# Kernel optimization log

Hardware: AMD Instinct MI355X
Metric: run time of the kernel (lower is better)

Reference implementation:

```python
import jax, jax.numpy as jnp
import numpy as np
import math

B, T, C, NH = 8, 1024, 768, 12
HD = C // NH
EPS = 1e-5

def layer_norm(x, g, b):
    mu = jnp.mean(x, axis=-1, keepdims=True)
    var = jnp.mean(jnp.square(x - mu), axis=-1, keepdims=True)
    return (x - mu) * jax.lax.rsqrt(var + EPS) * g + b

def setup_inputs() -> dict:
    key = jax.random.key(0)
    ks = jax.random.split(key, 10)
    s = lambda n: 1.0 / math.sqrt(n)
    return {
        "x": jax.random.normal(ks[0], (B, T, C), jnp.float32),
        "attn_mask": jax.random.randint(ks[1], (B, T), 0, 2, jnp.int32),
        "ln1_g": jnp.ones((C,), jnp.float32),
        "ln1_b": jnp.zeros((C,), jnp.float32),
        "W_attn": jax.random.normal(ks[2], (C, 3 * C), jnp.float32) * s(C),
        "b_attn": jnp.zeros((3 * C,), jnp.float32),
        "W_proj": jax.random.normal(ks[3], (C, C), jnp.float32) * s(C),
        "b_proj": jnp.zeros((C,), jnp.float32),
        "ln2_g": jnp.ones((C,), jnp.float32),
        "ln2_b": jnp.zeros((C,), jnp.float32),
        "W_fc": jax.random.normal(ks[4], (C, 4 * C), jnp.float32) * s(C),
        "b_fc": jnp.zeros((4 * C,), jnp.float32),
        "W_fc2": jax.random.normal(ks[5], (4 * C, C), jnp.float32) * s(4 * C),
        "b_fc2": jnp.zeros((C,), jnp.float32),
    }

def reference(x, attn_mask, ln1_g, ln1_b, W_attn, b_attn, W_proj, b_proj,
              ln2_g, ln2_b, W_fc, b_fc, W_fc2, b_fc2):
    # --- attention branch ---
    h = layer_norm(x, ln1_g, ln1_b)                     # [B,T,C]
    qkv = h @ W_attn + b_attn                           # [B,T,3C]
    q, k, v = jnp.split(qkv, 3, axis=-1)
    q = q.reshape(B, T, NH, HD).transpose(0, 2, 1, 3)   # [B,H,T,D]
    k = k.reshape(B, T, NH, HD).transpose(0, 2, 1, 3)
    v = v.reshape(B, T, NH, HD).transpose(0, 2, 1, 3)
    attn = jnp.einsum('bhqd,bhkd->bhqk', q, k) * (1.0 / math.sqrt(HD))
    mask = attn_mask[:, None, None, :]                  # [B,1,1,T] key-padding
    attn = jnp.where(mask == 0, -jnp.inf, attn)
    attn = jax.nn.softmax(attn, axis=-1)
    o = jnp.einsum('bhqk,bhkd->bhqd', attn, v)          # [B,H,T,D]
    o = o.transpose(0, 2, 1, 3).reshape(B, T, C)
    x = x + (o @ W_proj + b_proj)
    # --- MLP branch ---
    h2 = layer_norm(x, ln2_g, ln2_b)
    h2 = jax.nn.gelu(h2 @ W_fc + b_fc, approximate=True)
    x = x + (h2 @ W_fc2 + b_fc2)
    return x
```

## Files before the change

### kernel.cpp

```cpp
#include <hip/hip_runtime.h>
#include <hip/hip_bf16.h>
#include <math.h>

constexpr int kB  = 8;
constexpr int kT  = 1024;
constexpr int kC  = 768;
constexpr int kNH = 12;
constexpr int kHD = 64;
constexpr int kM  = kB * kT;
constexpr int k3C = 3 * kC;
constexpr int k4C = 4 * kC;

typedef __bf16 bf16x8 __attribute__((ext_vector_type(8)));
typedef float  f32x4  __attribute__((ext_vector_type(4)));
typedef unsigned short u16x8 __attribute__((ext_vector_type(8)));

__device__ inline void gload_lds16(const void* g, void* l) {
  __builtin_amdgcn_global_load_lds(
      (const __attribute__((address_space(1))) void*)g,
      (__attribute__((address_space(3))) void*)l, 16, 0, 0);
}

__device__ inline float ldx(const float* p) { return *p; }
__device__ inline float ldx(const __hip_bfloat16* p) { return __bfloat162float(*p); }

template <typename TIN>
__global__ __launch_bounds__(256) void ln_kernel(
    const TIN* __restrict__ x, const float* __restrict__ g,
    const float* __restrict__ bta, __hip_bfloat16* __restrict__ out)
{
  __shared__ float red[4];
  int row = blockIdx.x;
  int tid = threadIdx.x;
  const TIN* xr = x + (size_t)row * kC;
  float v0 = ldx(xr + tid), v1 = ldx(xr + tid + 256), v2 = ldx(xr + tid + 512);

  float s = v0 + v1 + v2;
#pragma unroll
  for (int off = 32; off; off >>= 1) s += __shfl_xor(s, off);
  if ((tid & 63) == 0) red[tid >> 6] = s;
  __syncthreads();
  float mu = (red[0] + red[1] + red[2] + red[3]) * (1.0f / kC);

  float d0 = v0 - mu, d1 = v1 - mu, d2 = v2 - mu;
  float q = d0 * d0 + d1 * d1 + d2 * d2;
#pragma unroll
  for (int off = 32; off; off >>= 1) q += __shfl_xor(q, off);
  __syncthreads();
  if ((tid & 63) == 0) red[tid >> 6] = q;
  __syncthreads();
  float var = (red[0] + red[1] + red[2] + red[3]) * (1.0f / kC);
  float inv = rsqrtf(var + 1e-5f);

  __hip_bfloat16* orow = out + (size_t)row * kC;
  orow[tid]       = __float2bfloat16(d0 * inv * g[tid]       + bta[tid]);
  orow[tid + 256] = __float2bfloat16(d1 * inv * g[tid + 256] + bta[tid + 256]);
  orow[tid + 512] = __float2bfloat16(d2 * inv * g[tid + 512] + bta[tid + 512]);
}

__global__ __launch_bounds__(256) void transpose_cast(
    const float* __restrict__ W, __hip_bfloat16* __restrict__ WT, int K, int N)
{
  __shared__ __hip_bfloat16 t[64][65];
  int k0 = blockIdx.y * 64, n0 = blockIdx.x * 64;
  int tid = threadIdx.x;
#pragma unroll
  for (int it = 0; it < 16; ++it) {
    int e = it * 256 + tid;
    int r = e >> 6, c = e & 63;
    t[r][c] = __float2bfloat16(W[(size_t)(k0 + r) * N + n0 + c]);
  }
  __syncthreads();
#pragma unroll
  for (int it = 0; it < 16; ++it) {
    int e = it * 256 + tid;
    int nr = e >> 6, kc = e & 63;
    WT[(size_t)(n0 + nr) * K + k0 + kc] = t[kc][nr];
  }
}

__global__ __launch_bounds__(256) void v_transpose(
    const __hip_bfloat16* __restrict__ qkv, __hip_bfloat16* __restrict__ vt)
{
  __shared__ __hip_bfloat16 tile[64][80];
  int b = blockIdx.z, h = blockIdx.y, t0 = blockIdx.x * 64;
  int tid = threadIdx.x;
  const __hip_bfloat16* vb = qkv + (size_t)(b * kT) * k3C + 2 * kC + h * kHD;
#pragma unroll
  for (int it = 0; it < 2; ++it) {
    int e = it * 256 + tid;
    int r = e >> 3, c8 = (e & 7) * 8;
    *(u16x8*)&tile[r][c8] = *(const u16x8*)(vb + (size_t)(t0 + r) * k3C + c8);
  }
  __syncthreads();
  __hip_bfloat16* vrow = vt + (size_t)(b * kNH + h) * kHD * kT;
#pragma unroll
  for (int it = 0; it < 2; ++it) {
    int e = it * 256 + tid;
    int d = e >> 3, k8 = (e & 7) * 8;
    u16x8 u;
#pragma unroll
    for (int m = 0; m < 8; ++m)
      u[m] = *(const unsigned short*)&tile[k8 + m][d];
    *(u16x8*)(vrow + (size_t)d * kT + t0 + k8) = u;
  }
}

__device__ inline float gelu_fast(float c) {
  float t = 0.7978845608028654f * (c + 0.044715f * c * c * c);
  float e = exp2f(t * 2.8853900817779268f);
  float th = 1.0f - 2.0f * __builtin_amdgcn_rcpf(e + 1.0f);
  return 0.5f * c * (1.0f + th);
}

template <int MODE>
__global__ __launch_bounds__(256) void gemm_bf16(
    const __hip_bfloat16* __restrict__ A,
    const __hip_bfloat16* __restrict__ WT,
    const float* __restrict__ bias,
    const void* __restrict__ Rv,
    void* __restrict__ outv, int M, int N, int K)
{
  __shared__ __align__(16) __hip_bfloat16 As[2][128 * 64];
  __shared__ __align__(16) __hip_bfloat16 Bs[2][128 * 64];
  const int tid  = threadIdx.x;
  const int lane = tid & 63, wid = tid >> 6;
  const int wr = wid >> 1, wc = wid & 1;
  const int r16 = lane & 15, g = lane >> 4;

  const int nwg = gridDim.x * gridDim.y;
  const int bid = blockIdx.y * gridDim.x + blockIdx.x;
  const int swz = (bid & 7) * (nwg >> 3) + (bid >> 3);
  const int m0 = (swz / gridDim.x) * 128;
  const int n0 = (swz % gridDim.x) * 128;

  const __hip_bfloat16* Abase = A  + (size_t)m0 * K;
  const __hip_bfloat16* Bbase = WT + (size_t)n0 * K;

  f32x4 acc[4][4] = {};

  auto stage = [&](int t, int buf) {
    const __hip_bfloat16* Ap = Abase + t * 64;
    const __hip_bfloat16* Bp = Bbase + t * 64;
#pragma unroll
    for (int it = 0; it < 4; ++it) {
      int e = it * 256 + tid;
      int row = e >> 3, ch = (e & 7) ^ (row & 7);
      char* la = (char*)&As[buf][0] + (it * 4096 + (tid & ~63) * 16);
      char* lb = (char*)&Bs[buf][0] + (it * 4096 + (tid & ~63) * 16);
      gload_lds16(Ap + (size_t)row * K + ch * 8, la);
      gload_lds16(Bp + (size_t)row * K + ch * 8, lb);
    }
  };

  auto compute = [&](const char* Ab, const char* Bb) {
#pragma unroll
    for (int s = 0; s < 2; ++s) {
      bf16x8 af[4], bf[4];
#pragma unroll
      for (int i = 0; i < 4; ++i) {
        int ar = wr * 64 + i * 16 + r16;
        af[i] = *(const bf16x8*)(Ab + ar * 128 + (((s * 4 + g) ^ (ar & 7)) << 4));
        int br = wc * 64 + i * 16 + r16;
        bf[i] = *(const bf16x8*)(Bb + br * 128 + (((s * 4 + g) ^ (br & 7)) << 4));
      }
#pragma unroll
      for (int i = 0; i < 4; ++i)
#pragma unroll
        for (int j = 0; j < 4; ++j)
          acc[i][j] = __builtin_amdgcn_mfma_f32_16x16x32_bf16(af[i], bf[j],
                                                              acc[i][j], 0, 0, 0);
    }
  };

  const int NT = K >> 6;
  stage(0, 0);
  __syncthreads();

  for (int t = 0; t < NT; t += 2) {
    stage(t + 1, 1);
    compute((const char*)&As[0][0], (const char*)&Bs[0][0]);
    __syncthreads();
    if (t + 2 < NT) stage(t + 2, 0);
    compute((const char*)&As[1][0], (const char*)&Bs[1][0]);
    __syncthreads();
  }

  const int r0 = m0 + wr * 64 + g * 4;
  const int c0 = n0 + wc * 64 + r16;
#pragma unroll
  for (int i = 0; i < 4; ++i) {
#pragma unroll
    for (int j = 0; j < 4; ++j) {
      int col = c0 + j * 16;
      float bv = bias[col];
#pragma unroll
      for (int q = 0; q < 4; ++q) {
        int row = r0 + i * 16 + q;
        float c = acc[i][j][q] + bv;
        if (MODE == 3) {
          c += ((const float*)Rv)[(size_t)row * N + col];
          ((__hip_bfloat16*)outv)[(size_t)row * N + col] = __float2bfloat16(c);
        } else if (MODE == 4) {
          c += __bfloat162float(((const __hip_bfloat16*)Rv)[(size_t)row * N + col]);
          ((float*)outv)[(size_t)row * N + col] = c;
        } else {
          if (MODE == 2) c = gelu_fast(c);
          ((__hip_bfloat16*)outv)[(size_t)row * N + col] = __float2bfloat16(c);
        }
      }
    }
  }
}

__global__ __launch_bounds__(256) void attn_mfma(
    const __hip_bfloat16* __restrict__ qkv,
    const __hip_bfloat16* __restrict__ vt,
    const int* __restrict__ mask,
    __hip_bfloat16* __restrict__ o)
{
  __shared__ __align__(16) __hip_bfloat16 Ks[2][64 * 64];
  __shared__ __align__(16) __hip_bfloat16 Vs[2][64 * 64];
  __shared__ __align__(16) __hip_bfloat16 Ps[4 * 16 * 64];

  const int b = blockIdx.z, h = blockIdx.y, q0 = blockIdx.x * 64;
  const int tid = threadIdx.x, lane = tid & 63, wid = tid >> 6;
  const int r16 = lane & 15, g = lane >> 4;
  const size_t rs = k3C;
  const __hip_bfloat16* qb = qkv + (size_t)(b * kT) * rs + h * kHD;
  const __hip_bfloat16* kb = qb + kC;
  const __hip_bfloat16* vtb = vt + (size_t)(b * kNH + h) * kHD * kT;
  const int* mrow = mask + b * kT;
  constexpr float kSc = 0.125f * 1.4426950408889634f;

  auto stage = [&](int t, int buf) {
#pragma unroll
    for (int it = 0; it < 2; ++it) {
      int e = it * 256 + tid;
      int row = e >> 3, ch = (e & 7) ^ (row & 7);
      char* lk = (char*)&Ks[buf][0] + (it * 4096 + (tid & ~63) * 16);
      char* lv = (char*)&Vs[buf][0] + (it * 4096 + (tid & ~63) * 16);
      gload_lds16(kb + (size_t)(t * 64 + row) * rs + ch * 8, lk);
      gload_lds16(vtb + (size_t)row * kT + t * 64 + ch * 8, lv);
    }
  };

  bf16x8 qf[2];
  {
    const __hip_bfloat16* qr = qb + (size_t)(q0 + wid * 16 + r16) * rs;
#pragma unroll
    for (int s = 0; s < 2; ++s) qf[s] = *(const bf16x8*)(qr + s * 32 + g * 8);
  }
  stage(0, 0);
  unsigned long long km = 0;
#pragma unroll
  for (int t = 0; t < 16; ++t)
#pragma unroll
    for (int j = 0; j < 4; ++j)
      if (mrow[t * 64 + 16 * j + r16] != 0)
        km |= 1ull << (t * 4 + j);
  __syncthreads();

  f32x4 o_acc[4] = {};
  float l_part[4] = {0.f, 0.f, 0.f, 0.f};
  __hip_bfloat16* Pw = Ps + wid * 1024;

  for (int t = 0; t < 16; ++t) {
    const int buf = t & 1;
    if (t + 1 < 16) stage(t + 1, buf ^ 1);

    const char* Kb = (const char*)&Ks[buf][0];
    const char* Vb = (const char*)&Vs[buf][0];

    f32x4 sa[4] = {};
#pragma unroll
    for (int j = 0; j < 4; ++j) {
#pragma unroll
      for (int s = 0; s < 2; ++s) {
        int kr = 16 * j + r16;
        bf16x8 kf = *(const bf16x8*)(Kb + kr * 128 +
                                     (((s * 4 + g) ^ (kr & 7)) << 4));
        sa[j] = __builtin_amdgcn_mfma_f32_16x16x32_bf16(qf[s], kf, sa[j], 0, 0, 0);
      }
    }

#pragma unroll
    for (int r = 0; r < 4; ++r) {
      float p[4];
#pragma unroll
      for (int j = 0; j < 4; ++j) {
        float pj = exp2f(sa[j][r] * kSc);
        p[j] = ((km >> (t * 4 + j)) & 1ull) ? pj : 0.f;
      }
      l_part[r] += (p[0] + p[1]) + (p[2] + p[3]);
      int q = g * 4 + r;
      char* pwq = (char*)Pw + q * 128 + (r16 & 7) * 2;
#pragma unroll
      for (int j = 0; j < 4; ++j) {
        int chn = ((j << 1) | (r16 >> 3)) ^ (q & 7);
        *(__hip_bfloat16*)(pwq + (chn << 4)) = __float2bfloat16(p[j]);
      }
    }

    asm volatile("s_waitcnt lgkmcnt(0)" ::: "memory");
    __builtin_amdgcn_sched_barrier(0);

#pragma unroll
    for (int s = 0; s < 2; ++s) {
      bf16x8 pf = *(const bf16x8*)((const char*)Pw + r16 * 128 +
                                   (((s * 4 + g) ^ (r16 & 7)) << 4));
#pragma unroll
      for (int db = 0; db < 4; ++db) {
        int vr = 16 * db + r16;
        bf16x8 vf = *(const bf16x8*)(Vb + vr * 128 +
                                     (((s * 4 + g) ^ (vr & 7)) << 4));
        o_acc[db] = __builtin_amdgcn_mfma_f32_16x16x32_bf16(pf, vf, o_acc[db], 0, 0, 0);
      }
    }
    __syncthreads();
  }

#pragma unroll
  for (int r = 0; r < 4; ++r) {
    float l = l_part[r];
#pragma unroll
    for (int off = 8; off; off >>= 1) l += __shfl_xor(l, off);
    float inv = 1.f / l;
    size_t row = (size_t)(b * kT) + q0 + wid * 16 + g * 4 + r;
#pragma unroll
    for (int db = 0; db < 4; ++db)
      o[row * kC + h * kHD + 16 * db + r16] = __float2bfloat16(o_acc[db][r] * inv);
  }
}

extern "C" void kernel_launch(void* const* d_in, const int* in_sizes, int n_in,
                              void* d_out, int out_size, void* d_ws, size_t ws_size,
                              hipStream_t stream) {
  const float* x      = (const float*)d_in[0];
  const int*   amask  = (const int*)  d_in[1];
  const float* ln1_g  = (const float*)d_in[2];
  const float* ln1_b  = (const float*)d_in[3];
  const float* W_attn = (const float*)d_in[4];
  const float* b_attn = (const float*)d_in[5];
  const float* W_proj = (const float*)d_in[6];
  const float* b_proj = (const float*)d_in[7];
  const float* ln2_g  = (const float*)d_in[8];
  const float* ln2_b  = (const float*)d_in[9];
  const float* W_fc   = (const float*)d_in[10];
  const float* b_fc   = (const float*)d_in[11];
  const float* W_fc2  = (const float*)d_in[12];
  const float* b_fc2  = (const float*)d_in[13];
  float* out = (float*)d_out;

  char* ws = (char*)d_ws;
  __hip_bfloat16* h_bf    = (__hip_bfloat16*)(ws);
  __hip_bfloat16* qkv_bf  = (__hip_bfloat16*)(ws + (size_t)16 * 1024 * 1024);
  __hip_bfloat16* fc_bf   = qkv_bf;
  __hip_bfloat16* wt_attn = (__hip_bfloat16*)(ws + (size_t)68 * 1024 * 1024);
  __hip_bfloat16* wt_proj = (__hip_bfloat16*)(ws + (size_t)72 * 1024 * 1024);
  __hip_bfloat16* wt_fc   = (__hip_bfloat16*)(ws + (size_t)74 * 1024 * 1024);
  __hip_bfloat16* wt_fc2  = (__hip_bfloat16*)(ws + (size_t)79 * 1024 * 1024);
  __hip_bfloat16* vt_bf   = (__hip_bfloat16*)(ws + (size_t)84 * 1024 * 1024);
  __hip_bfloat16* x1_bf   = vt_bf;

  dim3 blk(256);

  transpose_cast<<<dim3(k3C / 64, kC / 64), blk, 0, stream>>>(W_attn, wt_attn, kC, k3C);
  transpose_cast<<<dim3(kC / 64, kC / 64), blk, 0, stream>>>(W_proj, wt_proj, kC, kC);
  transpose_cast<<<dim3(k4C / 64, kC / 64), blk, 0, stream>>>(W_fc, wt_fc, kC, k4C);
  transpose_cast<<<dim3(kC / 64, k4C / 64), blk, 0, stream>>>(W_fc2, wt_fc2, k4C, kC);

  ln_kernel<float><<<kM, blk, 0, stream>>>(x, ln1_g, ln1_b, h_bf);
  gemm_bf16<0><<<dim3(k3C / 128, kM / 128), blk, 0, stream>>>(
      h_bf, wt_attn, b_attn, nullptr, qkv_bf, kM, k3C, kC);
  v_transpose<<<dim3(kT / 64, kNH, kB), blk, 0, stream>>>(qkv_bf, vt_bf);
  attn_mfma<<<dim3(kT / 64, kNH, kB), blk, 0, stream>>>(qkv_bf, vt_bf, amask, h_bf);
  gemm_bf16<3><<<dim3(kC / 128, kM / 128), blk, 0, stream>>>(
      h_bf, wt_proj, b_proj, x, x1_bf, kM, kC, kC);
  ln_kernel<__hip_bfloat16><<<kM, blk, 0, stream>>>(x1_bf, ln2_g, ln2_b, h_bf);
  gemm_bf16<2><<<dim3(k4C / 128, kM / 128), blk, 0, stream>>>(
      h_bf, wt_fc, b_fc, nullptr, fc_bf, kM, k4C, kC);
  gemm_bf16<4><<<dim3(kC / 128, kM / 128), blk, 0, stream>>>(
      fc_bf, wt_fc2, b_fc2, x1_bf, out, kM, kC, k4C);
}
```

Measured before the change: 287.0 us.

## Fuse V transpose into QKV GEMM epilogue and precompute attention addresses

The QKV GEMM is split in two: the first launch writes Q and K in the usual row-major layout, and a second launch (new MODE 5) writes V directly in the transposed [b,h,d,t] layout. This removes the separate v_transpose kernel and its extra read and write of V. The attention kernel also precomputes its global, LDS and P-buffer store addresses outside the loop, and applies the mask as an additive bias before exp2 instead of a select. The cost is an extra GEMM launch with 64-byte scattered stores in the V epilogue, and a qkv buffer whose V section is never written.

```diff
diff --git a/kernel.cpp b/kernel.cpp
--- a/kernel.cpp
+++ b/kernel.cpp
@@ -76,33 +76,6 @@
     int e = it * 256 + tid;
     int nr = e >> 6, kc = e & 63;
     WT[(size_t)(n0 + nr) * K + k0 + kc] = t[kc][nr];
-  }
-}
-
-__global__ __launch_bounds__(256) void v_transpose(
-    const __hip_bfloat16* __restrict__ qkv, __hip_bfloat16* __restrict__ vt)
-{
-  __shared__ __hip_bfloat16 tile[64][80];
-  int b = blockIdx.z, h = blockIdx.y, t0 = blockIdx.x * 64;
-  int tid = threadIdx.x;
-  const __hip_bfloat16* vb = qkv + (size_t)(b * kT) * k3C + 2 * kC + h * kHD;
-#pragma unroll
-  for (int it = 0; it < 2; ++it) {
-    int e = it * 256 + tid;
-    int r = e >> 3, c8 = (e & 7) * 8;
-    *(u16x8*)&tile[r][c8] = *(const u16x8*)(vb + (size_t)(t0 + r) * k3C + c8);
-  }
-  __syncthreads();
-  __hip_bfloat16* vrow = vt + (size_t)(b * kNH + h) * kHD * kT;
-#pragma unroll
-  for (int it = 0; it < 2; ++it) {
-    int e = it * 256 + tid;
-    int d = e >> 3, k8 = (e & 7) * 8;
-    u16x8 u;
-#pragma unroll
-    for (int m = 0; m < 8; ++m)
-      u[m] = *(const unsigned short*)&tile[k8 + m][d];
-    *(u16x8*)(vrow + (size_t)d * kT + t0 + k8) = u;
   }
 }
 
@@ -194,19 +167,32 @@
     for (int j = 0; j < 4; ++j) {
       int col = c0 + j * 16;
       float bv = bias[col];
-#pragma unroll
-      for (int q = 0; q < 4; ++q) {
-        int row = r0 + i * 16 + q;
-        float c = acc[i][j][q] + bv;
-        if (MODE == 3) {
-          c += ((const float*)Rv)[(size_t)row * N + col];
-          ((__hip_bfloat16*)outv)[(size_t)row * N + col] = __float2bfloat16(c);
-        } else if (MODE == 4) {
-          c += __bfloat162float(((const __hip_bfloat16*)Rv)[(size_t)row * N + col]);
-          ((float*)outv)[(size_t)row * N + col] = c;
-        } else {
-          if (MODE == 2) c = gelu_fast(c);
-          ((__hip_bfloat16*)outv)[(size_t)row * N + col] = __float2bfloat16(c);
+      if (MODE == 5) {
+        int hh = col >> 6, dd = col & 63;
+        int rowb = r0 + i * 16;
+        int bb = rowb >> 10, tr = rowb & 1023;
+        __hip_bfloat16 t4[4];
+#pragma unroll
+        for (int q = 0; q < 4; ++q)
+          t4[q] = __float2bfloat16(acc[i][j][q] + bv);
+        __hip_bfloat16* vp = (__hip_bfloat16*)outv +
+            ((size_t)(bb * kNH + hh) * kHD + dd) * kT + tr;
+        *(uint2*)vp = *(const uint2*)t4;
+      } else {
+#pragma unroll
+        for (int q = 0; q < 4; ++q) {
+          int row = r0 + i * 16 + q;
+          float c = acc[i][j][q] + bv;
+          if (MODE == 3) {
+            c += ((const float*)Rv)[(size_t)row * N + col];
+            ((__hip_bfloat16*)outv)[(size_t)row * N + col] = __float2bfloat16(c);
+          } else if (MODE == 4) {
+            c += __bfloat162float(((const __hip_bfloat16*)Rv)[(size_t)row * N + col]);
+            ((float*)outv)[(size_t)row * N + col] = c;
+          } else {
+            if (MODE == 2) c = gelu_fast(c);
+            ((__hip_bfloat16*)outv)[(size_t)row * N + col] = __float2bfloat16(c);
+          }
         }
       }
     }
@@ -233,25 +219,39 @@
   const int* mrow = mask + b * kT;
   constexpr float kSc = 0.125f * 1.4426950408889634f;
 
-  auto stage = [&](int t, int buf) {
-#pragma unroll
-    for (int it = 0; it < 2; ++it) {
-      int e = it * 256 + tid;
-      int row = e >> 3, ch = (e & 7) ^ (row & 7);
-      char* lk = (char*)&Ks[buf][0] + (it * 4096 + (tid & ~63) * 16);
-      char* lv = (char*)&Vs[buf][0] + (it * 4096 + (tid & ~63) * 16);
-      gload_lds16(kb + (size_t)(t * 64 + row) * rs + ch * 8, lk);
-      gload_lds16(vtb + (size_t)row * kT + t * 64 + ch * 8, lv);
-    }
-  };
-
+  const __hip_bfloat16* kg[2];
+  const __hip_bfloat16* vg[2];
+  char* lk[2][2]; char* lv[2][2];
+#pragma unroll
+  for (int it = 0; it < 2; ++it) {
+    int e = it * 256 + tid;
+    int row = e >> 3, ch = (e & 7) ^ (row & 7);
+    kg[it] = kb + (size_t)row * rs + ch * 8;
+    vg[it] = vtb + (size_t)row * kT + ch * 8;
+#pragma unroll
+    for (int buf = 0; buf < 2; ++buf) {
+      lk[buf][it] = (char*)&Ks[buf][0] + (it * 4096 + (tid & ~63) * 16);
+      lv[buf][it] = (char*)&Vs[buf][0] + (it * 4096 + (tid & ~63) * 16);
+    }
+  }
+  __hip_bfloat16* Pw = Ps + wid * 1024;
+  __hip_bfloat16* paddr[4][4];
+#pragma unroll
+  for (int r = 0; r < 4; ++r) {
+    int q = g * 4 + r;
+    char* pwq = (char*)Pw + q * 128 + (r16 & 7) * 2;
+#pragma unroll
+    for (int j = 0; j < 4; ++j) {
+      int chn = ((j << 1) | (r16 >> 3)) ^ (q & 7);
+      paddr[r][j] = (__hip_bfloat16*)(pwq + (chn << 4));
+    }
+  }
   bf16x8 qf[2];
   {
     const __hip_bfloat16* qr = qb + (size_t)(q0 + wid * 16 + r16) * rs;
 #pragma unroll
     for (int s = 0; s < 2; ++s) qf[s] = *(const bf16x8*)(qr + s * 32 + g * 8);
   }
-  stage(0, 0);
   unsigned long long km = 0;
 #pragma unroll
   for (int t = 0; t < 16; ++t)
@@ -259,15 +259,21 @@
     for (int j = 0; j < 4; ++j)
       if (mrow[t * 64 + 16 * j + r16] != 0)
         km |= 1ull << (t * 4 + j);
+
+  gload_lds16(kg[0], lk[0][0]); gload_lds16(vg[0], lv[0][0]);
+  gload_lds16(kg[1], lk[0][1]); gload_lds16(vg[1], lv[0][1]);
   __syncthreads();
 
   f32x4 o_acc[4] = {};
   float l_part[4] = {0.f, 0.f, 0.f, 0.f};
-  __hip_bfloat16* Pw = Ps + wid * 1024;
 
   for (int t = 0; t < 16; ++t) {
     const int buf = t & 1;
-    if (t + 1 < 16) stage(t + 1, buf ^ 1);
+    kg[0] += 64 * rs; kg[1] += 64 * rs; vg[0] += 64; vg[1] += 64;
+    if (t + 1 < 16) {
+      gload_lds16(kg[0], lk[buf ^ 1][0]); gload_lds16(vg[0], lv[buf ^ 1][0]);
+      gload_lds16(kg[1], lk[buf ^ 1][1]); gload_lds16(vg[1], lv[buf ^ 1][1]);
+    }
 
     const char* Kb = (const char*)&Ks[buf][0];
     const char* Vb = (const char*)&Vs[buf][0];
@@ -284,22 +290,20 @@
       }
     }
 
+    float mb[4];
+#pragma unroll
+    for (int j = 0; j < 4; ++j)
+      mb[j] = ((km >> (t * 4 + j)) & 1ull) ? 0.f : -20000.f;
 #pragma unroll
     for (int r = 0; r < 4; ++r) {
       float p[4];
 #pragma unroll
-      for (int j = 0; j < 4; ++j) {
-        float pj = exp2f(sa[j][r] * kSc);
-        p[j] = ((km >> (t * 4 + j)) & 1ull) ? pj : 0.f;
-      }
+      for (int j = 0; j < 4; ++j)
+        p[j] = exp2f(fmaf(sa[j][r], kSc, mb[j]));
       l_part[r] += (p[0] + p[1]) + (p[2] + p[3]);
-      int q = g * 4 + r;
-      char* pwq = (char*)Pw + q * 128 + (r16 & 7) * 2;
-#pragma unroll
-      for (int j = 0; j < 4; ++j) {
-        int chn = ((j << 1) | (r16 >> 3)) ^ (q & 7);
-        *(__hip_bfloat16*)(pwq + (chn << 4)) = __float2bfloat16(p[j]);
-      }
+#pragma unroll
+      for (int j = 0; j < 4; ++j)
+        *paddr[r][j] = __float2bfloat16(p[j]);
     }
 
     asm volatile("s_waitcnt lgkmcnt(0)" ::: "memory");
@@ -371,9 +375,11 @@
   transpose_cast<<<dim3(kC / 64, k4C / 64), blk, 0, stream>>>(W_fc2, wt_fc2, k4C, kC);
 
   ln_kernel<float><<<kM, blk, 0, stream>>>(x, ln1_g, ln1_b, h_bf);
-  gemm_bf16<0><<<dim3(k3C / 128, kM / 128), blk, 0, stream>>>(
+  gemm_bf16<0><<<dim3(12, kM / 128), blk, 0, stream>>>(
       h_bf, wt_attn, b_attn, nullptr, qkv_bf, kM, k3C, kC);
-  v_transpose<<<dim3(kT / 64, kNH, kB), blk, 0, stream>>>(qkv_bf, vt_bf);
+  gemm_bf16<5><<<dim3(6, kM / 128), blk, 0, stream>>>(
+      h_bf, wt_attn + (size_t)(2 * kC) * kC, b_attn + 2 * kC, nullptr,
+      vt_bf, kM, kC, kC);
   attn_mfma<<<dim3(kT / 64, kNH, kB), blk, 0, stream>>>(qkv_bf, vt_bf, amask, h_bf);
   gemm_bf16<3><<<dim3(kC / 128, kM / 128), blk, 0, stream>>>(
       h_bf, wt_proj, b_proj, x, x1_bf, kM, kC, kC);
```

After: 287.2 us. About the same (+0.1%).
